# Kernel tuning notes

Hardware: AMD Instinct MI355X
Metric: run time of the kernel (lower is better)

The kernel has to match this reference:

```python
import jax, jax.numpy as jnp
import numpy as np

B, S, D, H = 8, 1024, 1024, 16
HD = D // H  # head_dim = 64


def setup_inputs() -> dict:
    key = jax.random.key(0)
    ks = jax.random.split(key, 5)
    scale = 1.0 / np.sqrt(D)
    return {
        "x": jax.random.normal(ks[0], (B, S, D), dtype=jnp.float32),
        "wq": jax.random.normal(ks[1], (D, D), dtype=jnp.float32) * scale,
        "wk": jax.random.normal(ks[2], (D, D), dtype=jnp.float32) * scale,
        "wv": jax.random.normal(ks[3], (D, D), dtype=jnp.float32) * scale,
        "wo": jax.random.normal(ks[4], (D, D), dtype=jnp.float32) * scale,
    }


def reference(x, wq, wk, wv, wo):
    b, s, d = x.shape
    # nn.Linear: y = x @ W.T  (weights stored [out, in])
    q = (x @ wq.T).reshape(b, s, H, HD).transpose(0, 2, 1, 3)  # [b,h,s,hd]
    k = (x @ wk.T).reshape(b, s, H, HD).transpose(0, 2, 1, 3)
    v = (x @ wv.T).reshape(b, s, H, HD).transpose(0, 2, 1, 3)
    scores = jnp.einsum("bhqd,bhkd->bhqk", q, k) / jnp.sqrt(jnp.float32(HD))
    attn = jax.nn.softmax(scores, axis=-1)  # dropout p=0.0 -> identity
    out = jnp.einsum("bhqk,bhkd->bhqd", attn, v)
    out = out.transpose(0, 2, 1, 3).reshape(b, s, d)
    return out @ wo.T
```

## Files before the change

### kernel.cpp

```cpp
#include <hip/hip_runtime.h>
#include <hip/hip_bf16.h>
#include <math.h>

#define BB 8
#define SS 1024
#define DD 1024
#define HH 16
#define HDIM 64
#define MM (BB * SS)
#define QSCALE 0.1803368801111204f

typedef __attribute__((ext_vector_type(8))) short s8v;
typedef __attribute__((ext_vector_type(4))) short s4v;
typedef __attribute__((ext_vector_type(4))) float f4v;

#define GLD16(g, l)                                                            \
  __builtin_amdgcn_global_load_lds(                                            \
      (const __attribute__((address_space(1))) void*)(g),                      \
      (__attribute__((address_space(3))) void*)(l), 16, 0, 0)

#define BARRIER()                                                              \
  do {                                                                         \
    asm volatile("" ::: "memory");                                             \
    __builtin_amdgcn_s_barrier();                                              \
    asm volatile("" ::: "memory");                                             \
  } while (0)

__device__ __forceinline__ unsigned short bf16_ru(float f) {
  return (unsigned short)((__float_as_uint(f) + 0x8000u) >> 16);
}

__device__ __forceinline__ unsigned bf16_pack2(float f0, float f1) {
#if __has_builtin(__builtin_amdgcn_perm)
  unsigned a = __float_as_uint(f0) + 0x8000u;
  unsigned b = __float_as_uint(f1) + 0x8000u;
  return __builtin_amdgcn_perm(b, a, 0x07060302u);
#else
  return (unsigned)bf16_ru(f0) | ((unsigned)bf16_ru(f1) << 16);
#endif
}

__device__ __forceinline__ float fast_exp2(float x) {
  return __builtin_amdgcn_exp2f(x);
}

__global__ void cast_all(const float* __restrict__ x, const float* __restrict__ wq,
                         const float* __restrict__ wk, const float* __restrict__ wv,
                         const float* __restrict__ wo, __hip_bfloat16* __restrict__ xb,
                         __hip_bfloat16* __restrict__ wqkvb,
                         __hip_bfloat16* __restrict__ wob) {
  int blk = blockIdx.x;
  const float* src;
  __hip_bfloat16* dst;
  int base;
  if (blk < 2048) {
    src = x; dst = xb; base = blk * 4096;
  } else if (blk < 2304) {
    src = wq; dst = wqkvb; base = (blk - 2048) * 4096;
  } else if (blk < 2560) {
    src = wk; dst = wqkvb + (1 << 20); base = (blk - 2304) * 4096;
  } else if (blk < 2816) {
    src = wv; dst = wqkvb + (2 << 20); base = (blk - 2560) * 4096;
  } else {
    src = wo; dst = wob; base = (blk - 2816) * 4096;
  }
#pragma unroll
  for (int it = 0; it < 4; ++it) {
    int idx = base + it * 1024 + threadIdx.x * 4;
    float4 f = *(const float4*)&src[idx];
    *(uint2*)&dst[idx] = uint2{bf16_pack2(f.x, f.y), bf16_pack2(f.z, f.w)};
  }
}

__global__ __launch_bounds__(512, 2) void gemm_qk8(
    const __hip_bfloat16* __restrict__ A, const __hip_bfloat16* __restrict__ Bm,
    __hip_bfloat16* __restrict__ Qo, __hip_bfloat16* __restrict__ Ko) {
  __shared__ char smem[131072];

  const int tid = threadIdx.x;
  const int wave = tid >> 6;
  const int lane = tid & 63;
  const int l15 = lane & 15;
  const int quad = lane >> 4;
  const int c8 = lane & 7;
  const int r8 = lane >> 3;

  const int id = blockIdx.y * 8 + blockIdx.x;
  const int nid = (id & 7) * 32 + (id >> 3);
  const int m0 = (nid >> 3) * 256;
  const int n0 = (nid & 7) * 256;

  const int wm = (wave >> 2) * 128;
  const int wn = (wave & 3) * 64;

  auto stA = [&](int t, int r) {
    const int row = r * 64 + wave * 8 + r8;
    const int sc = (c8 ^ (row & 7)) * 8;
    GLD16(A + (size_t)(m0 + row) * DD + t * 64 + sc,
          smem + (t & 1) * 65536 + (r * 64 + wave * 8) * 128);
  };
  auto stB = [&](int t, int r) {
    const int row = r * 64 + wave * 8 + r8;
    const int sc = (c8 ^ (row & 7)) * 8;
    GLD16(Bm + (size_t)(n0 + row) * DD + t * 64 + sc,
          smem + (t & 1) * 65536 + 32768 + (r * 64 + wave * 8) * 128);
  };

  f4v acc[8][4];
#pragma unroll
  for (int i = 0; i < 8; ++i)
#pragma unroll
    for (int j = 0; j < 4; ++j) acc[i][j] = {0.f, 0.f, 0.f, 0.f};

  stB(0, 0); stB(0, 1);
  stB(0, 2); stB(0, 3);
  stA(0, 0); stA(0, 2);
  stA(0, 1); stA(0, 3);
  stB(1, 0); stB(1, 1);
  stB(1, 2); stB(1, 3);
  asm volatile("s_waitcnt vmcnt(6)" ::: "memory");
  BARRIER();

  for (int t = 0; t < 16; ++t) {
    char* bufA = smem + (t & 1) * 65536;
    char* bufB = bufA + 32768;
    s8v bfr[2][4];
    s8v af[4];

#pragma unroll
    for (int kk = 0; kk < 2; ++kk)
#pragma unroll
      for (int j = 0; j < 4; ++j)
        bfr[kk][j] = *(const s8v*)(bufB + (size_t)(wn + j * 16 + l15) * 128 +
                                   (((kk * 4 + quad) ^ (l15 & 7)) << 4));
#pragma unroll
    for (int mi = 0; mi < 4; ++mi)
      af[mi] = *(const s8v*)(bufA + (size_t)(wm + mi * 16 + l15) * 128 +
                             ((quad ^ (l15 & 7)) << 4));
    if (t < 15) { stA(t + 1, 0); stA(t + 1, 2); }
    BARRIER();
    __builtin_amdgcn_s_setprio(1);
#pragma unroll
    for (int mi = 0; mi < 4; ++mi)
#pragma unroll
      for (int j = 0; j < 4; ++j)
        acc[mi][j] = __builtin_amdgcn_mfma_f32_16x16x32_bf16(bfr[0][j], af[mi],
                                                             acc[mi][j], 0, 0, 0);
    __builtin_amdgcn_s_setprio(0);
    if (t == 15) asm volatile("s_waitcnt vmcnt(0)" ::: "memory");
    else         asm volatile("s_waitcnt vmcnt(6)" ::: "memory");
    BARRIER();

#pragma unroll
    for (int mi = 0; mi < 4; ++mi)
      af[mi] = *(const s8v*)(bufA + (size_t)(wm + 64 + mi * 16 + l15) * 128 +
                             ((quad ^ (l15 & 7)) << 4));
    if (t < 15) { stA(t + 1, 1); stA(t + 1, 3); }
    BARRIER();
    __builtin_amdgcn_s_setprio(1);
#pragma unroll
    for (int mi = 0; mi < 4; ++mi)
#pragma unroll
      for (int j = 0; j < 4; ++j)
        acc[4 + mi][j] = __builtin_amdgcn_mfma_f32_16x16x32_bf16(
            bfr[0][j], af[mi], acc[4 + mi][j], 0, 0, 0);
    __builtin_amdgcn_s_setprio(0);
    BARRIER();

#pragma unroll
    for (int mi = 0; mi < 4; ++mi)
      af[mi] = *(const s8v*)(bufA + (size_t)(wm + mi * 16 + l15) * 128 +
                             (((4 + quad) ^ (l15 & 7)) << 4));
    if (t < 14) { stB(t + 2, 0); stB(t + 2, 1); }
    BARRIER();
    __builtin_amdgcn_s_setprio(1);
#pragma unroll
    for (int mi = 0; mi < 4; ++mi)
#pragma unroll
      for (int j = 0; j < 4; ++j)
        acc[mi][j] = __builtin_amdgcn_mfma_f32_16x16x32_bf16(bfr[1][j], af[mi],
                                                             acc[mi][j], 0, 0, 0);
    __builtin_amdgcn_s_setprio(0);
    BARRIER();

#pragma unroll
    for (int mi = 0; mi < 4; ++mi)
      af[mi] = *(const s8v*)(bufA + (size_t)(wm + 64 + mi * 16 + l15) * 128 +
                             (((4 + quad) ^ (l15 & 7)) << 4));
    if (t < 14) { stB(t + 2, 2); stB(t + 2, 3); }
    BARRIER();
    __builtin_amdgcn_s_setprio(1);
#pragma unroll
    for (int mi = 0; mi < 4; ++mi)
#pragma unroll
      for (int j = 0; j < 4; ++j)
        acc[4 + mi][j] = __builtin_amdgcn_mfma_f32_16x16x32_bf16(
            bfr[1][j], af[mi], acc[4 + mi][j], 0, 0, 0);
    __builtin_amdgcn_s_setprio(0);
    if (t < 14)       asm volatile("s_waitcnt vmcnt(6)" ::: "memory");
    else if (t == 14) asm volatile("s_waitcnt vmcnt(2)" ::: "memory");
    BARRIER();
  }

  const bool isQ = (n0 < 1024);
  const float scl = isQ ? QSCALE : 1.0f;
  const int h = ((n0 + wn) & 1023) >> 6;
  const int sb = m0 + wm;
  const int b = sb >> 10, s0 = sb & 1023;
  char* epc = smem + wave * 16384;
#pragma unroll
  for (int i = 0; i < 8; ++i) {
#pragma unroll
    for (int j = 0; j < 4; ++j) {
      const int r = i * 16 + l15;
      const int c0 = j * 16 + quad * 4;
      const int off = r * 128 + (((c0 >> 3) ^ (r & 7)) << 4) + ((c0 & 7) * 2);
      *(uint2*)(epc + off) =
          uint2{bf16_pack2(acc[i][j][0] * scl, acc[i][j][1] * scl),
                bf16_pack2(acc[i][j][2] * scl, acc[i][j][3] * scl)};
    }
  }
  asm volatile("s_waitcnt lgkmcnt(0)" ::: "memory");
  __hip_bfloat16* dst = (isQ ? Qo : Ko) + ((size_t)(b * HH + h) * SS + s0) * HDIM;
#pragma unroll
  for (int it = 0; it < 16; ++it) {
    const int r = it * 8 + r8;
    uint4 vv = *(const uint4*)(epc + r * 128 + (((lane & 7) ^ r8) << 4));
    *(uint4*)&dst[(size_t)r * HDIM + (lane & 7) * 8] = vv;
  }
}

template <int MODE>
__global__ __launch_bounds__(256, 3) void gemm_bt(
    const __hip_bfloat16* __restrict__ A, const __hip_bfloat16* __restrict__ Bm,
    float* __restrict__ Cf, __hip_bfloat16* __restrict__ Qo,
    __hip_bfloat16* __restrict__ Ko, __hip_bfloat16* __restrict__ Vt) {
  __shared__ __hip_bfloat16 smem[2][128 * 64];
  __hip_bfloat16* sA = smem[0];
  __hip_bfloat16* sB = smem[1];

  const int tid = threadIdx.x;
  const int wave = tid >> 6;
  const int lane = tid & 63;
  const int l15 = lane & 15;
  const int quad = lane >> 4;
  const int c8 = lane & 7;
  const int r8 = lane >> 3;

  constexpr int GX = 8;
  constexpr int NWG = GX * 64;
  const int id = blockIdx.y * GX + blockIdx.x;
  const int nid = (id & 7) * (NWG / 8) + (id >> 3);
  const int m0 = (nid / GX) * 128;
  const int n0 = (nid % GX) * 128;

  const int wm = (wave >> 1) * 64;
  const int wn = (wave & 1) * 64;

  f4v acc[4][4];
#pragma unroll
  for (int i = 0; i < 4; ++i)
#pragma unroll
    for (int j = 0; j < 4; ++j) acc[i][j] = {0.f, 0.f, 0.f, 0.f};

  for (int kt = 0; kt < DD / 64; ++kt) {
    const int k0 = kt * 64;
    __syncthreads();
#pragma unroll
    for (int r = 0; r < 4; ++r) {
      int rb = r * 32 + wave * 8;
      int row = rb + r8;
      int scol = (c8 ^ (row & 7)) * 8;
      GLD16(A + (size_t)(m0 + row) * DD + k0 + scol, &sA[rb * 64]);
      GLD16(Bm + (size_t)(n0 + row) * DD + k0 + scol, &sB[rb * 64]);
    }
    __syncthreads();

#pragma unroll
    for (int kk = 0; kk < 2; ++kk) {
      s8v af[4], bf[4];
#pragma unroll
      for (int i = 0; i < 4; ++i)
        af[i] = *(const s8v*)&sA[(wm + i * 16 + l15) * 64 +
                                 (((kk * 4 + quad) ^ (l15 & 7)) * 8)];
#pragma unroll
      for (int j = 0; j < 4; ++j)
        bf[j] = *(const s8v*)&sB[(wn + j * 16 + l15) * 64 +
                                 (((kk * 4 + quad) ^ (l15 & 7)) * 8)];
#pragma unroll
      for (int i = 0; i < 4; ++i)
#pragma unroll
        for (int j = 0; j < 4; ++j)
          acc[i][j] = (MODE == 2)
                          ? __builtin_amdgcn_mfma_f32_16x16x32_bf16(af[i], bf[j],
                                                                    acc[i][j], 0, 0, 0)
                          : __builtin_amdgcn_mfma_f32_16x16x32_bf16(bf[j], af[i],
                                                                    acc[i][j], 0, 0, 0);
    }
  }

  if constexpr (MODE == 1) {
#pragma unroll
    for (int i = 0; i < 4; ++i) {
#pragma unroll
      for (int j = 0; j < 4; ++j) {
        const int s_abs = m0 + wm + i * 16 + l15;
        const int col = n0 + wn + j * 16 + quad * 4;
        float4 f4 = {acc[i][j][0], acc[i][j][1], acc[i][j][2], acc[i][j][3]};
        *(float4*)&Cf[(size_t)s_abs * DD + col] = f4;
      }
    }
  } else {
    __syncthreads();
    char* epc = (char*)smem + wave * 8192;
#pragma unroll
    for (int i = 0; i < 4; ++i) {
#pragma unroll
      for (int j = 0; j < 4; ++j) {
        const int r = j * 16 + l15;
        const int c0 = i * 16 + quad * 4;
        const int off = r * 128 + (((c0 >> 3) ^ (r & 7)) << 4) + ((c0 & 7) * 2);
        *(uint2*)(epc + off) = uint2{bf16_pack2(acc[i][j][0], acc[i][j][1]),
                                     bf16_pack2(acc[i][j][2], acc[i][j][3])};
      }
    }
    asm volatile("s_waitcnt lgkmcnt(0)" ::: "memory");
    const int rr8 = lane >> 3;
    const int ch = (lane & 7) ^ rr8;
    const int h = ((n0 + wn) & 1023) >> 6;
    const int sb = m0 + wm;
    const int b = sb >> 10, s0 = sb & 1023;
    __hip_bfloat16* dst = Vt + (size_t)(b * HH + h) * HDIM * SS + s0;
#pragma unroll
    for (int it = 0; it < 8; ++it) {
      const int r = it * 8 + rr8;
      uint4 vv = *(const uint4*)(epc + r * 128 + ch * 16);
      *(uint4*)&dst[(size_t)r * SS + (lane & 7) * 8] = vv;
    }
  }
}

#define KPLD 76
__global__ __launch_bounds__(256, 4) void attn_kernel(
    const __hip_bfloat16* __restrict__ Q, const __hip_bfloat16* __restrict__ K,
    const __hip_bfloat16* __restrict__ Vt, __hip_bfloat16* __restrict__ Oout) {
  __shared__ __hip_bfloat16 sK[64 * 64];
  __shared__ __hip_bfloat16 sVt[64 * 64];
  __shared__ unsigned short sP[4 * 32 * KPLD];

  const int tid = threadIdx.x;
  const int wave = tid >> 6;
  const int lane = tid & 63;
  const int l15 = lane & 15;
  const int quad = lane >> 4;
  const int c8 = lane & 7;
  const int r8 = lane >> 3;

  const int bh = blockIdx.x;
  const int q0 = blockIdx.y * 128;
  const size_t head = (size_t)bh * SS * HDIM;

  unsigned short* sPw = &sP[wave * 32 * KPLD];

  s8v qf[2][2];
#pragma unroll
  for (int mf = 0; mf < 2; ++mf) {
    int s = q0 + wave * 32 + mf * 16 + l15;
#pragma unroll
    for (int kk = 0; kk < 2; ++kk)
      qf[mf][kk] = *(const s8v*)&Q[head + (size_t)s * HDIM + kk * 32 + quad * 8];
  }

  s8v onesB;
#pragma unroll
  for (int j = 0; j < 8; ++j) onesB[j] = (short)0x3F80;

  f4v o[2][4];
  f4v lacc[2];
#pragma unroll
  for (int mf = 0; mf < 2; ++mf) {
    lacc[mf] = {0.f, 0.f, 0.f, 0.f};
#pragma unroll
    for (int f = 0; f < 4; ++f) o[mf][f] = {0.f, 0.f, 0.f, 0.f};
  }

  for (int kb = 0; kb < SS / 64; ++kb) {
    __syncthreads();
#pragma unroll
    for (int r = 0; r < 2; ++r) {
      int rb = r * 32 + wave * 8;
      int row = rb + r8;
      int sc8 = (c8 ^ (row & 7)) * 8;
      GLD16(&K[head + (size_t)(kb * 64 + row) * HDIM + sc8], &sK[rb * 64]);
      GLD16(&Vt[head + (size_t)row * SS + kb * 64 + sc8], &sVt[rb * 64]);
    }
    __syncthreads();

    f4v sc[2][4];
#pragma unroll
    for (int mf = 0; mf < 2; ++mf)
#pragma unroll
      for (int f = 0; f < 4; ++f) sc[mf][f] = {0.f, 0.f, 0.f, 0.f};
#pragma unroll
    for (int kk = 0; kk < 2; ++kk) {
#pragma unroll
      for (int f = 0; f < 4; ++f) {
        s8v kf = *(const s8v*)&sK[(f * 16 + l15) * 64 +
                                  (((kk * 4 + quad) ^ (l15 & 7)) * 8)];
#pragma unroll
        for (int mf = 0; mf < 2; ++mf)
          sc[mf][f] =
              __builtin_amdgcn_mfma_f32_16x16x32_bf16(kf, qf[mf][kk], sc[mf][f], 0, 0, 0);
      }
    }

#pragma unroll
    for (int mf = 0; mf < 2; ++mf)
#pragma unroll
      for (int f = 0; f < 4; ++f) {
        float p0 = fast_exp2(sc[mf][f][0]), p1 = fast_exp2(sc[mf][f][1]);
        float p2 = fast_exp2(sc[mf][f][2]), p3 = fast_exp2(sc[mf][f][3]);
        *(uint2*)&sPw[(mf * 16 + l15) * KPLD + f * 16 + quad * 4] =
            uint2{bf16_pack2(p0, p1), bf16_pack2(p2, p3)};
      }

#pragma unroll
    for (int kk = 0; kk < 2; ++kk) {
      s8v pf[2];
#pragma unroll
      for (int mf = 0; mf < 2; ++mf) {
        const unsigned short* p = &sPw[(mf * 16 + l15) * KPLD + kk * 32 + quad * 8];
        s4v lo = *(const s4v*)p;
        s4v hi = *(const s4v*)(p + 4);
        pf[mf] = __builtin_shufflevector(lo, hi, 0, 1, 2, 3, 4, 5, 6, 7);
        lacc[mf] = __builtin_amdgcn_mfma_f32_16x16x32_bf16(pf[mf], onesB, lacc[mf], 0, 0, 0);
      }
#pragma unroll
      for (int f = 0; f < 4; ++f) {
        s8v vf = *(const s8v*)&sVt[(f * 16 + l15) * 64 +
                                   (((kk * 4 + quad) ^ (l15 & 7)) * 8)];
#pragma unroll
        for (int mf = 0; mf < 2; ++mf)
          o[mf][f] =
              __builtin_amdgcn_mfma_f32_16x16x32_bf16(pf[mf], vf, o[mf][f], 0, 0, 0);
      }
    }
  }

  const int b = bh >> 4, h = bh & 15;
  char* epw = (char*)sPw;
#pragma unroll
  for (int mf = 0; mf < 2; ++mf) {
    float rl[4];
#pragma unroll
    for (int r = 0; r < 4; ++r) rl[r] = 1.0f / lacc[mf][r];
#pragma unroll
    for (int f = 0; f < 4; ++f)
#pragma unroll
      for (int r = 0; r < 4; ++r) {
        const int row = mf * 16 + quad * 4 + r;
        const int off =
            row * 128 + (((2 * f + (l15 >> 3)) ^ (row & 7)) << 4) + ((l15 & 7) * 2);
        *(unsigned short*)(epw + off) = bf16_ru(o[mf][f][r] * rl[r]);
      }
  }
  asm volatile("s_waitcnt lgkmcnt(0)" ::: "memory");
  const int rr8 = lane >> 3;
  unsigned short* dstO = (unsigned short*)Oout +
                         (size_t)(b * SS + q0 + wave * 32) * DD + h * HDIM;
#pragma unroll
  for (int it = 0; it < 4; ++it) {
    const int row = it * 8 + rr8;
    uint4 vv = *(const uint4*)(epw + row * 128 + (((lane & 7) ^ rr8) << 4));
    *(uint4*)&dstO[(size_t)row * DD + (lane & 7) * 8] = vv;
  }
}

extern "C" void kernel_launch(void* const* d_in, const int* in_sizes, int n_in,
                              void* d_out, int out_size, void* d_ws, size_t ws_size,
                              hipStream_t stream) {
  const float* x = (const float*)d_in[0];
  const float* wq = (const float*)d_in[1];
  const float* wk = (const float*)d_in[2];
  const float* wv = (const float*)d_in[3];
  const float* wo = (const float*)d_in[4];

  char* ws = (char*)d_ws;
  __hip_bfloat16* xb = (__hip_bfloat16*)(ws);
  __hip_bfloat16* wqkvb = (__hip_bfloat16*)(ws + (16 << 20));
  __hip_bfloat16* wob = (__hip_bfloat16*)(ws + (22 << 20));
  __hip_bfloat16* qh = (__hip_bfloat16*)(ws + (24 << 20));
  __hip_bfloat16* kh = (__hip_bfloat16*)(ws + (40 << 20));
  __hip_bfloat16* vt = (__hip_bfloat16*)(ws + (56 << 20));
  __hip_bfloat16* attnO = (__hip_bfloat16*)(ws + (72 << 20));

  cast_all<<<3072, 256, 0, stream>>>(x, wq, wk, wv, wo, xb, wqkvb, wob);

  gemm_qk8<<<dim3(8, 32), 512, 0, stream>>>(xb, wqkvb, qh, kh);
  gemm_bt<2><<<dim3(8, 64), 256, 0, stream>>>(xb, wqkvb + (2 << 20), nullptr,
                                              nullptr, nullptr, vt);

  attn_kernel<<<dim3(BB * HH, SS / 128), 256, 0, stream>>>(qh, kh, vt, attnO);

  gemm_bt<1><<<dim3(8, 64), 256, 0, stream>>>(attnO, wob, (float*)d_out, nullptr,
                                              nullptr, nullptr);
}
```

Measured before the change: 211.9 us.

## Replace V and output-projection GEMMs with 8-wave 256x128 double-buffered pipelined kernel

The V projection and output projection GEMMs move from a 4-wave 128x128 tile with synchronous per-k-step loading to an 8-wave 256x128 tile that double-buffers LDS. Loads for the next A tile and the B tile two steps ahead are issued while MFMAs run on the current buffer, with s_setprio raised around the MFMA blocks. This aims to hide global-to-LDS latency and to reuse each B tile across more rows. The cost is 96KB of LDS per block, which limits occupancy to about two blocks per CU, and more complex barrier and vmcnt bookkeeping.

```diff
diff --git a/kernel.cpp b/kernel.cpp
--- a/kernel.cpp
+++ b/kernel.cpp
@@ -230,14 +230,11 @@
   }
 }
 
-template <int MODE>
-__global__ __launch_bounds__(256, 3) void gemm_bt(
+template <bool SWAP>
+__global__ __launch_bounds__(512, 2) void gemm_np8(
     const __hip_bfloat16* __restrict__ A, const __hip_bfloat16* __restrict__ Bm,
-    float* __restrict__ Cf, __hip_bfloat16* __restrict__ Qo,
-    __hip_bfloat16* __restrict__ Ko, __hip_bfloat16* __restrict__ Vt) {
-  __shared__ __hip_bfloat16 smem[2][128 * 64];
-  __hip_bfloat16* sA = smem[0];
-  __hip_bfloat16* sB = smem[1];
+    float* __restrict__ Cf, __hip_bfloat16* __restrict__ Vt) {
+  __shared__ char smem[98304];
 
   const int tid = threadIdx.x;
   const int wave = tid >> 6;
@@ -247,59 +244,91 @@
   const int c8 = lane & 7;
   const int r8 = lane >> 3;
 
-  constexpr int GX = 8;
-  constexpr int NWG = GX * 64;
-  const int id = blockIdx.y * GX + blockIdx.x;
-  const int nid = (id & 7) * (NWG / 8) + (id >> 3);
-  const int m0 = (nid / GX) * 128;
-  const int n0 = (nid % GX) * 128;
+  const int id = blockIdx.y * 8 + blockIdx.x;
+  const int nid = (id & 7) * 32 + (id >> 3);
+  const int m0 = (nid >> 3) * 256;
+  const int n0 = (nid & 7) * 128;
 
   const int wm = (wave >> 1) * 64;
   const int wn = (wave & 1) * 64;
 
+  auto stA = [&](int t, int r) {
+    const int row = r * 64 + wave * 8 + r8;
+    const int sc = (c8 ^ (row & 7)) * 8;
+    GLD16(A + (size_t)(m0 + row) * DD + t * 64 + sc,
+          smem + (t & 1) * 49152 + (r * 64 + wave * 8) * 128);
+  };
+  auto stB = [&](int t, int r) {
+    const int row = r * 64 + wave * 8 + r8;
+    const int sc = (c8 ^ (row & 7)) * 8;
+    GLD16(Bm + (size_t)(n0 + row) * DD + t * 64 + sc,
+          smem + (t & 1) * 49152 + 32768 + (r * 64 + wave * 8) * 128);
+  };
+
   f4v acc[4][4];
 #pragma unroll
   for (int i = 0; i < 4; ++i)
 #pragma unroll
     for (int j = 0; j < 4; ++j) acc[i][j] = {0.f, 0.f, 0.f, 0.f};
 
-  for (int kt = 0; kt < DD / 64; ++kt) {
-    const int k0 = kt * 64;
-    __syncthreads();
-#pragma unroll
-    for (int r = 0; r < 4; ++r) {
-      int rb = r * 32 + wave * 8;
-      int row = rb + r8;
-      int scol = (c8 ^ (row & 7)) * 8;
-      GLD16(A + (size_t)(m0 + row) * DD + k0 + scol, &sA[rb * 64]);
-      GLD16(Bm + (size_t)(n0 + row) * DD + k0 + scol, &sB[rb * 64]);
-    }
-    __syncthreads();
-
-#pragma unroll
-    for (int kk = 0; kk < 2; ++kk) {
-      s8v af[4], bf[4];
-#pragma unroll
-      for (int i = 0; i < 4; ++i)
-        af[i] = *(const s8v*)&sA[(wm + i * 16 + l15) * 64 +
-                                 (((kk * 4 + quad) ^ (l15 & 7)) * 8)];
-#pragma unroll
-      for (int j = 0; j < 4; ++j)
-        bf[j] = *(const s8v*)&sB[(wn + j * 16 + l15) * 64 +
-                                 (((kk * 4 + quad) ^ (l15 & 7)) * 8)];
-#pragma unroll
-      for (int i = 0; i < 4; ++i)
-#pragma unroll
-        for (int j = 0; j < 4; ++j)
-          acc[i][j] = (MODE == 2)
-                          ? __builtin_amdgcn_mfma_f32_16x16x32_bf16(af[i], bf[j],
-                                                                    acc[i][j], 0, 0, 0)
-                          : __builtin_amdgcn_mfma_f32_16x16x32_bf16(bf[j], af[i],
-                                                                    acc[i][j], 0, 0, 0);
-    }
-  }
-
-  if constexpr (MODE == 1) {
+  stA(0, 0); stA(0, 1); stA(0, 2); stA(0, 3);
+  stB(0, 0); stB(0, 1);
+  stB(1, 0); stB(1, 1);
+  asm volatile("s_waitcnt vmcnt(2)" ::: "memory");
+  BARRIER();
+
+  for (int t = 0; t < 16; ++t) {
+    char* bufA = smem + (t & 1) * 49152;
+    char* bufB = bufA + 32768;
+    s8v bfr[2][4];
+    s8v af[4];
+
+#pragma unroll
+    for (int kk = 0; kk < 2; ++kk)
+#pragma unroll
+      for (int j = 0; j < 4; ++j)
+        bfr[kk][j] = *(const s8v*)(bufB + (size_t)(wn + j * 16 + l15) * 128 +
+                                   (((kk * 4 + quad) ^ (l15 & 7)) << 4));
+#pragma unroll
+    for (int mi = 0; mi < 4; ++mi)
+      af[mi] = *(const s8v*)(bufA + (size_t)(wm + mi * 16 + l15) * 128 +
+                             ((quad ^ (l15 & 7)) << 4));
+    if (t < 15) { stA(t + 1, 0); stA(t + 1, 1); stA(t + 1, 2); stA(t + 1, 3); }
+    BARRIER();
+    __builtin_amdgcn_s_setprio(1);
+#pragma unroll
+    for (int mi = 0; mi < 4; ++mi)
+#pragma unroll
+      for (int j = 0; j < 4; ++j)
+        acc[mi][j] = SWAP ? __builtin_amdgcn_mfma_f32_16x16x32_bf16(
+                                bfr[0][j], af[mi], acc[mi][j], 0, 0, 0)
+                          : __builtin_amdgcn_mfma_f32_16x16x32_bf16(
+                                af[mi], bfr[0][j], acc[mi][j], 0, 0, 0);
+    __builtin_amdgcn_s_setprio(0);
+    BARRIER();
+
+#pragma unroll
+    for (int mi = 0; mi < 4; ++mi)
+      af[mi] = *(const s8v*)(bufA + (size_t)(wm + mi * 16 + l15) * 128 +
+                             (((4 + quad) ^ (l15 & 7)) << 4));
+    if (t < 14) { stB(t + 2, 0); stB(t + 2, 1); }
+    BARRIER();
+    __builtin_amdgcn_s_setprio(1);
+#pragma unroll
+    for (int mi = 0; mi < 4; ++mi)
+#pragma unroll
+      for (int j = 0; j < 4; ++j)
+        acc[mi][j] = SWAP ? __builtin_amdgcn_mfma_f32_16x16x32_bf16(
+                                bfr[1][j], af[mi], acc[mi][j], 0, 0, 0)
+                          : __builtin_amdgcn_mfma_f32_16x16x32_bf16(
+                                af[mi], bfr[1][j], acc[mi][j], 0, 0, 0);
+    __builtin_amdgcn_s_setprio(0);
+    if (t < 14)       asm volatile("s_waitcnt vmcnt(2)" ::: "memory");
+    else if (t == 14) asm volatile("s_waitcnt vmcnt(0)" ::: "memory");
+    BARRIER();
+  }
+
+  if constexpr (SWAP) {
 #pragma unroll
     for (int i = 0; i < 4; ++i) {
 #pragma unroll
@@ -311,8 +340,7 @@
       }
     }
   } else {
-    __syncthreads();
-    char* epc = (char*)smem + wave * 8192;
+    char* epc = smem + wave * 8192;
 #pragma unroll
     for (int i = 0; i < 4; ++i) {
 #pragma unroll
@@ -325,15 +353,14 @@
       }
     }
     asm volatile("s_waitcnt lgkmcnt(0)" ::: "memory");
-    const int rr8 = lane >> 3;
-    const int ch = (lane & 7) ^ rr8;
+    const int ch = (lane & 7) ^ r8;
     const int h = ((n0 + wn) & 1023) >> 6;
     const int sb = m0 + wm;
     const int b = sb >> 10, s0 = sb & 1023;
     __hip_bfloat16* dst = Vt + (size_t)(b * HH + h) * HDIM * SS + s0;
 #pragma unroll
     for (int it = 0; it < 8; ++it) {
-      const int r = it * 8 + rr8;
+      const int r = it * 8 + r8;
       uint4 vv = *(const uint4*)(epc + r * 128 + ch * 16);
       *(uint4*)&dst[(size_t)r * SS + (lane & 7) * 8] = vv;
     }
@@ -497,11 +524,11 @@
   cast_all<<<3072, 256, 0, stream>>>(x, wq, wk, wv, wo, xb, wqkvb, wob);
 
   gemm_qk8<<<dim3(8, 32), 512, 0, stream>>>(xb, wqkvb, qh, kh);
-  gemm_bt<2><<<dim3(8, 64), 256, 0, stream>>>(xb, wqkvb + (2 << 20), nullptr,
-                                              nullptr, nullptr, vt);
+  gemm_np8<false><<<dim3(8, 32), 512, 0, stream>>>(xb, wqkvb + (2 << 20),
+                                                   nullptr, vt);
 
   attn_kernel<<<dim3(BB * HH, SS / 128), 256, 0, stream>>>(qh, kh, vt, attnO);
 
-  gemm_bt<1><<<dim3(8, 64), 256, 0, stream>>>(attnO, wob, (float*)d_out, nullptr,
-                                              nullptr, nullptr);
-}
+  gemm_np8<true><<<dim3(8, 32), 512, 0, stream>>>(attnO, wob, (float*)d_out,
+                                                  nullptr);
+}
```

New measurement: 216.3 us. +2.1%, slower.
